# Optimization experiments

Measured on AMD Instinct MI355X. Metric: run time of the kernel, lower is better.

The kernel has to match this reference:

```python
import jax, jax.numpy as jnp
import numpy as np

N = 65536          # total nodes (512 graphs x 128 nodes)
E = 524288         # edges
B = 512            # graphs
D_IN = 128
H_ENC = 256
LAT = 64
H_DEC = 512
NMAX = 128
NP = NMAX * (NMAX - 1) // 2   # 8128 upper-tri pairs
NSTATS = 7
BN_EPS = 1e-5


def _lin(k, i, o):
    return jax.random.normal(k, (i, o), jnp.float32) / np.sqrt(i).astype(np.float32), jnp.zeros((o,), jnp.float32)


def setup_inputs() -> dict:
    key = jax.random.key(0)
    ks = jax.random.split(key, 24)
    inp = {}
    inp['x'] = jax.random.normal(ks[0], (N, D_IN), jnp.float32)
    inp['edge_index'] = jax.random.randint(ks[1], (2, E), 0, N)
    inp['batch'] = jnp.arange(N) // NMAX
    inp['stats'] = jax.random.normal(ks[2], (B, NSTATS), jnp.float32)
    u = jax.random.uniform(ks[3], (B, NP, 2), jnp.float32, 1e-9, 1.0)
    inp['gumbel'] = -jnp.log(-jnp.log(u))
    # GIN conv params (3 layers): Linear -> LeakyReLU -> BN -> Linear -> LeakyReLU
    dims = [(D_IN, H_ENC), (H_ENC, H_ENC), (H_ENC, H_ENC)]
    for li, (di, do) in enumerate(dims):
        w1, b1 = _lin(ks[4 + 2 * li], di, do)
        w2, b2 = _lin(ks[5 + 2 * li], do, do)
        inp[f'cw1_{li}'], inp[f'cb1_{li}'] = w1, b1
        inp[f'cg_{li}'], inp[f'cbe_{li}'] = jnp.ones((do,), jnp.float32), jnp.zeros((do,), jnp.float32)
        inp[f'cw2_{li}'], inp[f'cb2_{li}'] = w2, b2
    # encoder head: BN(hidden+7) -> fc(hidden+7 -> hidden) -> fc_mu(hidden -> latent)
    inp['bn_g'] = jnp.ones((H_ENC + NSTATS,), jnp.float32)
    inp['bn_b'] = jnp.zeros((H_ENC + NSTATS,), jnp.float32)
    inp['fc_w'], inp['fc_b'] = _lin(ks[10], H_ENC + NSTATS, H_ENC)
    inp['mu_w'], inp['mu_b'] = _lin(ks[11], H_ENC, LAT)
    # decoder MLP: (latent+7) -> H_DEC -> H_DEC -> 2*NP
    inp['d0_w'], inp['d0_b'] = _lin(ks[12], LAT + NSTATS, H_DEC)
    inp['d1_w'], inp['d1_b'] = _lin(ks[13], H_DEC, H_DEC)
    inp['d2_w'], inp['d2_b'] = _lin(ks[14], H_DEC, 2 * NP)
    return inp


def _bn_eval(h, g, b):
    # BatchNorm1d in eval mode with default running stats (mean=0, var=1)
    return h * (g / jnp.sqrt(1.0 + BN_EPS)) + b


def _lrelu(h):
    return jnp.where(h > 0, h, 0.2 * h)


def reference(x, edge_index, batch, stats, gumbel,
              cw1_0, cb1_0, cg_0, cbe_0, cw2_0, cb2_0,
              cw1_1, cb1_1, cg_1, cbe_1, cw2_1, cb2_1,
              cw1_2, cb1_2, cg_2, cbe_2, cw2_2, cb2_2,
              bn_g, bn_b, fc_w, fc_b, mu_w, mu_b,
              d0_w, d0_b, d1_w, d1_b, d2_w, d2_b):
    src, dst = edge_index[0], edge_index[1]
    convs = [(cw1_0, cb1_0, cg_0, cbe_0, cw2_0, cb2_0),
             (cw1_1, cb1_1, cg_1, cbe_1, cw2_1, cb2_1),
             (cw1_2, cb1_2, cg_2, cbe_2, cw2_2, cb2_2)]
    h = x
    for w1, b1, g, be, w2, b2 in convs:
        # GINConv (eps=0): nn(x_i + sum_{j->i} x_j) via scatter-add on targets
        agg = h + jax.ops.segment_sum(h[src], dst, num_segments=N)
        t = _lrelu(agg @ w1 + b1)
        t = _bn_eval(t, g, be)
        h = _lrelu(t @ w2 + b2)
        # dropout inactive (eval mode)
    pooled = jax.ops.segment_sum(h, batch, num_segments=B)         # global_add_pool -> [B, H_ENC]
    out = jnp.concatenate([pooled, stats], axis=1)                 # [B, H_ENC+7]
    out = _bn_eval(out, bn_g, bn_b) @ fc_w + fc_b                  # [B, H_ENC]
    mu = out @ mu_w + mu_b                                         # reparameterize (eval) -> mu, [B, LAT]
    z = jnp.concatenate([mu, stats], axis=1)                       # [B, LAT+7] matches decoder input dim
    d = jax.nn.relu(z @ d0_w + d0_b)
    d = jax.nn.relu(d @ d1_w + d1_b)
    logits = (d @ d2_w + d2_b).reshape(B, NP, 2)
    # hard gumbel-softmax (tau=1) with straight-through, keep channel 0
    y = logits + gumbel
    soft = jax.nn.softmax(y, axis=-1)
    hard = jax.nn.one_hot(jnp.argmax(y, axis=-1), 2, dtype=soft.dtype)
    st = hard + soft - jax.lax.stop_gradient(soft)
    vals = st[:, :, 0]                                             # [B, NP]
    iu0, iu1 = jnp.triu_indices(NMAX, k=1)
    adj = jnp.zeros((B, NMAX, NMAX), vals.dtype).at[:, iu0, iu1].set(vals)
    adj = adj + jnp.swapaxes(adj, 1, 2)
    return adj
```

## Files before the change

### kernel.cpp

```cpp
#include <hip/hip_runtime.h>

#define NN 65536
#define NE 524288
#define BG 512
#define DIN 128
#define HE 256
#define LATD 64
#define HD 512
#define NMX 128
#define NPAIR 8128
#define NST 7

__global__ void vae_hist(const int* __restrict__ dst, int* __restrict__ cnt) {
    int e = blockIdx.x * 256 + threadIdx.x;
    if (e < NE) atomicAdd(&cnt[dst[e]], 1);
}

__global__ void vae_scan1(const int* __restrict__ cnt, int* __restrict__ excl, int* __restrict__ bsum) {
    __shared__ int sd[256];
    const int b = blockIdx.x, t = threadIdx.x;
    int v = cnt[b * 256 + t];
    sd[t] = v;
    __syncthreads();
    int acc = v;
    for (int off = 1; off < 256; off <<= 1) {
        int tv = (t >= off) ? sd[t - off] : 0;
        __syncthreads();
        acc += tv;
        sd[t] = acc;
        __syncthreads();
    }
    excl[b * 256 + t] = acc - v;
    if (t == 255) bsum[b] = acc;
}

__global__ void vae_scan2(int* __restrict__ bsum) {
    __shared__ int sd[256];
    const int t = threadIdx.x;
    int v = bsum[t];
    sd[t] = v;
    __syncthreads();
    int acc = v;
    for (int off = 1; off < 256; off <<= 1) {
        int tv = (t >= off) ? sd[t - off] : 0;
        __syncthreads();
        acc += tv;
        sd[t] = acc;
        __syncthreads();
    }
    bsum[t] = acc - v;
}

__global__ void vae_scan3(const int* __restrict__ excl, const int* __restrict__ bsum,
                          int* __restrict__ rs, int* __restrict__ cur) {
    const int i = blockIdx.x * 256 + threadIdx.x;
    const int v = excl[i] + bsum[blockIdx.x];
    rs[i] = v;
    cur[i] = v;
    if (i == NN - 1) rs[NN] = NE;
}

__global__ void vae_fill(const int* __restrict__ dst, int* __restrict__ cur, int* __restrict__ eid) {
    int e = blockIdx.x * 256 + threadIdx.x;
    if (e < NE) {
        int p = atomicAdd(&cur[dst[e]], 1);
        eid[p] = e;
    }
}

__global__ void vae_sort(const int* __restrict__ rs, int* __restrict__ eid,
                         const int* __restrict__ srcarr, int* __restrict__ csrc) {
    int n = blockIdx.x * 256 + threadIdx.x;
    if (n >= NN) return;
    int s = rs[n], e = rs[n + 1];
    for (int a = s + 1; a < e; ++a) {
        int key = eid[a];
        int b = a - 1;
        while (b >= s && eid[b] > key) { eid[b + 1] = eid[b]; --b; }
        eid[b + 1] = key;
    }
    for (int a = s; a < e; ++a) csrc[a] = srcarr[eid[a]];
}

template <int D>
__global__ __launch_bounds__(256) void vae_agg(const float* __restrict__ H,
                                               const int* __restrict__ csrc,
                                               const int* __restrict__ rs,
                                               float* __restrict__ Agg) {
    constexpr int LPG = D / 4;
    const int gid = blockIdx.x * 256 + threadIdx.x;
    const int node = gid / LPG;
    const int lane = gid % LPG;
    if (node >= NN) return;
    float4 acc = *reinterpret_cast<const float4*>(H + (size_t)node * D + lane * 4);
    const int s = rs[node], e = rs[node + 1];
    for (int a = s; a < e; ++a) {
        float4 v = *reinterpret_cast<const float4*>(H + (size_t)csrc[a] * D + lane * 4);
        acc.x += v.x; acc.y += v.y; acc.z += v.z; acc.w += v.w;
    }
    *reinterpret_cast<float4*>(Agg + (size_t)node * D + lane * 4) = acc;
}

template <int K, int EPI>
__global__ __launch_bounds__(256, 2) void vae_sgemm(const float* __restrict__ A,
                                                    const float* __restrict__ W,
                                                    const float* __restrict__ bias,
                                                    const float* __restrict__ g,
                                                    const float* __restrict__ be,
                                                    float* __restrict__ Out) {
    __shared__ float As[32][132];
    __shared__ float Bs[32][264];
    const int tid = threadIdx.x;
    const int tx = tid & 15, ty = tid >> 4;
    const int rowBlk = blockIdx.x * 128;

    float acc[8][16];
#pragma unroll
    for (int r = 0; r < 8; r++)
#pragma unroll
        for (int c = 0; c < 16; c++) acc[r][c] = 0.f;

    const int arow = tid >> 1;
    const int ak = (tid & 1) * 16;
    const float* aptr = A + (size_t)(rowBlk + arow) * K + ak;
    const float* bptr = W + (size_t)ty * HE + tx * 4;

    float4 pa0, pa1, pa2, pa3;
    float4 pb0, pb1, pb2, pb3, pb4, pb5, pb6, pb7;
    auto gload = [&](int ck) {
        const float* an = aptr + ck * 32;
        pa0 = *reinterpret_cast<const float4*>(an);
        pa1 = *reinterpret_cast<const float4*>(an + 4);
        pa2 = *reinterpret_cast<const float4*>(an + 8);
        pa3 = *reinterpret_cast<const float4*>(an + 12);
        const float* bn0 = bptr + (size_t)(ck * 32) * HE;
        pb0 = *reinterpret_cast<const float4*>(bn0);
        pb1 = *reinterpret_cast<const float4*>(bn0 + 64);
        pb2 = *reinterpret_cast<const float4*>(bn0 + 128);
        pb3 = *reinterpret_cast<const float4*>(bn0 + 192);
        const float* bn1 = bn0 + 16 * HE;
        pb4 = *reinterpret_cast<const float4*>(bn1);
        pb5 = *reinterpret_cast<const float4*>(bn1 + 64);
        pb6 = *reinterpret_cast<const float4*>(bn1 + 128);
        pb7 = *reinterpret_cast<const float4*>(bn1 + 192);
    };
    auto swrite = [&]() {
        As[ak + 0][arow] = pa0.x;  As[ak + 1][arow] = pa0.y;
        As[ak + 2][arow] = pa0.z;  As[ak + 3][arow] = pa0.w;
        As[ak + 4][arow] = pa1.x;  As[ak + 5][arow] = pa1.y;
        As[ak + 6][arow] = pa1.z;  As[ak + 7][arow] = pa1.w;
        As[ak + 8][arow] = pa2.x;  As[ak + 9][arow] = pa2.y;
        As[ak + 10][arow] = pa2.z; As[ak + 11][arow] = pa2.w;
        As[ak + 12][arow] = pa3.x; As[ak + 13][arow] = pa3.y;
        As[ak + 14][arow] = pa3.z; As[ak + 15][arow] = pa3.w;
        *reinterpret_cast<float4*>(&Bs[ty][tx * 4]) = pb0;
        *reinterpret_cast<float4*>(&Bs[ty][tx * 4 + 64]) = pb1;
        *reinterpret_cast<float4*>(&Bs[ty][tx * 4 + 128]) = pb2;
        *reinterpret_cast<float4*>(&Bs[ty][tx * 4 + 192]) = pb3;
        *reinterpret_cast<float4*>(&Bs[ty + 16][tx * 4]) = pb4;
        *reinterpret_cast<float4*>(&Bs[ty + 16][tx * 4 + 64]) = pb5;
        *reinterpret_cast<float4*>(&Bs[ty + 16][tx * 4 + 128]) = pb6;
        *reinterpret_cast<float4*>(&Bs[ty + 16][tx * 4 + 192]) = pb7;
    };

    constexpr int NCK = K / 32;
    gload(0);
    for (int ck = 0; ck < NCK; ++ck) {
        __syncthreads();
        swrite();
        __syncthreads();
        if (ck + 1 < NCK) gload(ck + 1);
#pragma unroll 16
        for (int k = 0; k < 32; ++k) {
            float4 a0 = *reinterpret_cast<const float4*>(&As[k][ty * 8]);
            float4 a1 = *reinterpret_cast<const float4*>(&As[k][ty * 8 + 4]);
            float4 b0 = *reinterpret_cast<const float4*>(&Bs[k][tx * 4]);
            float4 b1 = *reinterpret_cast<const float4*>(&Bs[k][tx * 4 + 64]);
            float4 b2 = *reinterpret_cast<const float4*>(&Bs[k][tx * 4 + 128]);
            float4 b3 = *reinterpret_cast<const float4*>(&Bs[k][tx * 4 + 192]);
            float ar[8] = {a0.x, a0.y, a0.z, a0.w, a1.x, a1.y, a1.z, a1.w};
            float bv[16] = {b0.x, b0.y, b0.z, b0.w, b1.x, b1.y, b1.z, b1.w,
                            b2.x, b2.y, b2.z, b2.w, b3.x, b3.y, b3.z, b3.w};
#pragma unroll
            for (int r = 0; r < 8; r++)
#pragma unroll
                for (int c = 0; c < 16; c++)
                    acc[r][c] = fmaf(ar[r], bv[c], acc[r][c]);
        }
    }

    if constexpr (EPI == 2) {
        float psum[16];
#pragma unroll
        for (int c = 0; c < 16; c++) psum[c] = 0.f;
#pragma unroll
        for (int cg = 0; cg < 4; cg++) {
            const int col = cg * 64 + tx * 4;
            float4 bb = *reinterpret_cast<const float4*>(&bias[col]);
            float bbv[4] = {bb.x, bb.y, bb.z, bb.w};
#pragma unroll
            for (int r = 0; r < 8; r++)
#pragma unroll
                for (int c = 0; c < 4; c++) {
                    float t = acc[r][cg * 4 + c] + bbv[c];
                    t = t > 0.f ? t : 0.2f * t;
                    psum[cg * 4 + c] += t;
                }
        }
        __syncthreads();
#pragma unroll
        for (int cg = 0; cg < 4; cg++)
#pragma unroll
            for (int c = 0; c < 4; c++)
                Bs[ty][cg * 64 + tx * 4 + c] = psum[cg * 4 + c];
        __syncthreads();
        float s = 0.f;
#pragma unroll
        for (int k = 0; k < 16; k++) s += Bs[k][tid];
        Out[(size_t)blockIdx.x * HE + tid] = s;
        return;
    }

    const float sq = sqrtf(1.0f + 1e-5f);
#pragma unroll
    for (int cg = 0; cg < 4; cg++) {
        const int col = cg * 64 + tx * 4;
        float4 bb = *reinterpret_cast<const float4*>(&bias[col]);
        float bbv[4] = {bb.x, bb.y, bb.z, bb.w};
        float sc[4], bev[4];
        if constexpr (EPI == 0) {
            float4 gg = *reinterpret_cast<const float4*>(&g[col]);
            float4 ee = *reinterpret_cast<const float4*>(&be[col]);
            sc[0] = gg.x / sq; sc[1] = gg.y / sq; sc[2] = gg.z / sq; sc[3] = gg.w / sq;
            bev[0] = ee.x; bev[1] = ee.y; bev[2] = ee.z; bev[3] = ee.w;
        }
#pragma unroll
        for (int r = 0; r < 8; r++) {
            const int row = rowBlk + ty * 8 + r;
            float o[4];
#pragma unroll
            for (int c = 0; c < 4; c++) {
                float t = acc[r][cg * 4 + c] + bbv[c];
                t = t > 0.f ? t : 0.2f * t;
                if constexpr (EPI == 0) t = t * sc[c] + bev[c];
                o[c] = t;
            }
            *reinterpret_cast<float4*>(Out + (size_t)row * HE + col) =
                *reinterpret_cast<float4*>(&o[0]);
        }
    }
}

__global__ __launch_bounds__(256) void vae_pooldec(const float* __restrict__ pooled, const float* __restrict__ stats,
                                                   const float* __restrict__ bng, const float* __restrict__ bnb,
                                                   const float* __restrict__ fcw, const float* __restrict__ fcb,
                                                   const float* __restrict__ muw, const float* __restrict__ mub,
                                                   const float* __restrict__ d0w, const float* __restrict__ d0b,
                                                   const float* __restrict__ d1w, const float* __restrict__ d1b,
                                                   float* __restrict__ Dm) {
    __shared__ float vin[264];
    __shared__ float fo[256];
    __shared__ float z[72];
    __shared__ float dd[512];
    const int b = blockIdx.x, t = threadIdx.x;

    const float sq = sqrtf(1.0f + 1e-5f);
    float m0 = pooled[(size_t)b * HE + t] * (bng[t] / sq) + bnb[t];
    vin[t] = m0;
    if (t < NST) vin[HE + t] = stats[b * NST + t] * (bng[HE + t] / sq) + bnb[HE + t];
    __syncthreads();

    float a = fcb[t];
    for (int k = 0; k < HE + NST; k++) a = fmaf(vin[k], fcw[(size_t)k * HE + t], a);
    fo[t] = a;
    __syncthreads();

    if (t < LATD) {
        float m = mub[t];
        for (int k = 0; k < HE; k++) m = fmaf(fo[k], muw[(size_t)k * LATD + t], m);
        z[t] = m;
    }
    if (t >= LATD && t < LATD + NST) z[t] = stats[b * NST + (t - LATD)];
    __syncthreads();

    float a0 = d0b[t], a1 = d0b[t + 256];
    for (int k = 0; k < LATD + NST; k++) {
        float zk = z[k];
        a0 = fmaf(zk, d0w[(size_t)k * HD + t], a0);
        a1 = fmaf(zk, d0w[(size_t)k * HD + t + 256], a1);
    }
    dd[t] = a0 > 0.f ? a0 : 0.f;
    dd[t + 256] = a1 > 0.f ? a1 : 0.f;
    __syncthreads();

    float c0 = d1b[t], c1 = d1b[t + 256];
    for (int k = 0; k < HD; k++) {
        float dk = dd[k];
        c0 = fmaf(dk, d1w[(size_t)k * HD + t], c0);
        c1 = fmaf(dk, d1w[(size_t)k * HD + t + 256], c1);
    }
    Dm[(size_t)b * HD + t] = c0 > 0.f ? c0 : 0.f;
    Dm[(size_t)b * HD + t + 256] = c1 > 0.f ? c1 : 0.f;
}

__global__ void vae_pairdiff(const float* __restrict__ In, float* __restrict__ Od) {
    int gidx = blockIdx.x * 256 + threadIdx.x;
    int r = gidx >> 11, pq = gidx & 2047;
    float4 o;
    o.x = 0.f; o.y = 0.f; o.z = 0.f; o.w = 0.f;
    if (pq < 2032) {
        const float* s = In + (size_t)r * (2 * NPAIR) + pq * 8;
        float4 u = *reinterpret_cast<const float4*>(s);
        float4 v = *reinterpret_cast<const float4*>(s + 4);
        o.x = u.x - u.y; o.y = u.z - u.w; o.z = v.x - v.y; o.w = v.z - v.w;
    }
    *reinterpret_cast<float4*>(Od + (size_t)r * 8192 + pq * 4) = o;
}

__global__ __launch_bounds__(256, 4) void vae_d2gemm(const float* __restrict__ A,
                                                     const float* __restrict__ Wd,
                                                     const float* __restrict__ Bb,
                                                     float* __restrict__ Gd) {
    __shared__ float As[16][132];
    __shared__ float Bs[16][68];
    const int tid = threadIdx.x;
    const int tx = tid & 15, ty = tid >> 4;
    const int rowBlk = blockIdx.y * 128, colBlk = blockIdx.x * 64;

    float acc[8][4];
#pragma unroll
    for (int r = 0; r < 8; r++)
#pragma unroll
        for (int c = 0; c < 4; c++) acc[r][c] = 0.f;

    const int arow = tid >> 1;
    const int ak = (tid & 1) * 8;
    const float* aptr = A + (size_t)(rowBlk + arow) * HD + ak;
    const int bk = tid >> 4;
    const int bc = (tid & 15) * 4;
    const float* bptr = Wd + (size_t)bk * 8192 + colBlk + bc;

    float4 pa0 = *reinterpret_cast<const float4*>(aptr);
    float4 pa1 = *reinterpret_cast<const float4*>(aptr + 4);
    float4 pb = *reinterpret_cast<const float4*>(bptr);

    constexpr int NCK = HD / 16;
    for (int ck = 0; ck < NCK; ++ck) {
        __syncthreads();
        As[ak + 0][arow] = pa0.x;
        As[ak + 1][arow] = pa0.y;
        As[ak + 2][arow] = pa0.z;
        As[ak + 3][arow] = pa0.w;
        As[ak + 4][arow] = pa1.x;
        As[ak + 5][arow] = pa1.y;
        As[ak + 6][arow] = pa1.z;
        As[ak + 7][arow] = pa1.w;
        *reinterpret_cast<float4*>(&Bs[bk][bc]) = pb;
        __syncthreads();
        if (ck + 1 < NCK) {
            const float* an = aptr + (ck + 1) * 16;
            pa0 = *reinterpret_cast<const float4*>(an);
            pa1 = *reinterpret_cast<const float4*>(an + 4);
            pb = *reinterpret_cast<const float4*>(bptr + (size_t)(ck + 1) * 16 * 8192);
        }
#pragma unroll
        for (int k = 0; k < 16; ++k) {
            float4 a0 = *reinterpret_cast<const float4*>(&As[k][ty * 8]);
            float4 a1 = *reinterpret_cast<const float4*>(&As[k][ty * 8 + 4]);
            float4 b = *reinterpret_cast<const float4*>(&Bs[k][tx * 4]);
            float ar[8] = {a0.x, a0.y, a0.z, a0.w, a1.x, a1.y, a1.z, a1.w};
            float bv[4] = {b.x, b.y, b.z, b.w};
#pragma unroll
            for (int r = 0; r < 8; r++)
#pragma unroll
                for (int c = 0; c < 4; c++)
                    acc[r][c] = fmaf(ar[r], bv[c], acc[r][c]);
        }
    }

    const int col = colBlk + tx * 4;
    if (col < NPAIR) {
        const float* bp = Bb + 2 * col;
        float4 u = *reinterpret_cast<const float4*>(bp);
        float4 v = *reinterpret_cast<const float4*>(bp + 4);
        float bd[4] = {u.x - u.y, u.z - u.w, v.x - v.y, v.z - v.w};
#pragma unroll
        for (int r = 0; r < 8; r++) {
            const int b_ = rowBlk + ty * 8 + r;
            float* gp = Gd + (size_t)b_ * 8192 + col;
            float4 gv = *reinterpret_cast<const float4*>(gp);
            float gvv[4] = {gv.x, gv.y, gv.z, gv.w};
            float o[4];
#pragma unroll
            for (int c = 0; c < 4; c++) {
                float y = acc[r][c] + bd[c] + gvv[c];
                o[c] = (y >= 0.f) ? 1.0f : 0.0f;
            }
            *reinterpret_cast<float4*>(gp) = *reinterpret_cast<float4*>(&o[0]);
        }
    }
}

__global__ __launch_bounds__(256) void vae_scatter(const float* __restrict__ vals, float* __restrict__ Out) {
    __shared__ float sv[8192];
    const int b = blockIdx.x, t = threadIdx.x;
    const float* vp = vals + (size_t)b * 8192;
#pragma unroll
    for (int i = 0; i < 8; ++i)
        *reinterpret_cast<float4*>(&sv[(i * 256 + t) * 4]) =
            *reinterpret_cast<const float4*>(&vp[(i * 256 + t) * 4]);
    __syncthreads();
    float* op = Out + (size_t)b * (NMX * NMX);
#pragma unroll
    for (int it = 0; it < 16; ++it) {
        int pos = (it * 256 + t) * 4;
        int i = pos >> 7, j0 = pos & 127;
        float o[4];
#pragma unroll
        for (int e = 0; e < 4; ++e) {
            int j = j0 + e;
            float v;
            if (i == j) v = 0.f;
            else if (i < j) v = sv[((i * (255 - i)) >> 1) + j - i - 1];
            else v = sv[((j * (255 - j)) >> 1) + i - j - 1];
            o[e] = v;
        }
        *reinterpret_cast<float4*>(&op[pos]) = *reinterpret_cast<float4*>(&o[0]);
    }
}

extern "C" void kernel_launch(void* const* d_in, const int* in_sizes, int n_in,
                              void* d_out, int out_size, void* d_ws, size_t ws_size,
                              hipStream_t stream) {
    const float* x = (const float*)d_in[0];
    const int* ei = (const int*)d_in[1];
    const float* stats = (const float*)d_in[3];
    const float* gum = (const float*)d_in[4];
    const float* cw1[3] = {(const float*)d_in[5], (const float*)d_in[11], (const float*)d_in[17]};
    const float* cb1[3] = {(const float*)d_in[6], (const float*)d_in[12], (const float*)d_in[18]};
    const float* cg[3] = {(const float*)d_in[7], (const float*)d_in[13], (const float*)d_in[19]};
    const float* cbe[3] = {(const float*)d_in[8], (const float*)d_in[14], (const float*)d_in[20]};
    const float* cw2[3] = {(const float*)d_in[9], (const float*)d_in[15], (const float*)d_in[21]};
    const float* cb2[3] = {(const float*)d_in[10], (const float*)d_in[16], (const float*)d_in[22]};
    const float* bng = (const float*)d_in[23];
    const float* bnb = (const float*)d_in[24];
    const float* fcw = (const float*)d_in[25];
    const float* fcb = (const float*)d_in[26];
    const float* muw = (const float*)d_in[27];
    const float* mub = (const float*)d_in[28];
    const float* d0w = (const float*)d_in[29];
    const float* d0b = (const float*)d_in[30];
    const float* d1w = (const float*)d_in[31];
    const float* d1b = (const float*)d_in[32];
    const float* d2w = (const float*)d_in[33];
    const float* d2b = (const float*)d_in[34];
    float* Out = (float*)d_out;

    char* wp = (char*)d_ws;
    auto alloc = [&](size_t bytes) -> void* {
        void* p = (void*)wp;
        wp += (bytes + 255) & ~(size_t)255;
        return p;
    };
    float* hA = (float*)alloc((size_t)NN * HE * 4);
    float* hB = (float*)alloc((size_t)NN * HE * 4);
    int* cnt = (int*)alloc((size_t)NN * 4);
    int* rs = (int*)alloc((size_t)(NN + 64) * 4);
    int* cur = (int*)alloc((size_t)NN * 4);
    int* eid = (int*)alloc((size_t)NE * 4);
    int* csrc = (int*)alloc((size_t)NE * 4);
    int* bsum = (int*)alloc((size_t)256 * 4);
    float* Dm = (float*)alloc((size_t)BG * HD * 4);
    float* pooled = (float*)alloc((size_t)BG * HE * 4);

    float* wdiff = hA;
    float* gdiff = hA + (size_t)HD * 8192;

    const int* srcArr = ei;
    const int* dstArr = ei + NE;

    hipMemsetAsync(cnt, 0, (size_t)NN * 4, stream);
    vae_hist<<<NE / 256, 256, 0, stream>>>(dstArr, cnt);
    vae_scan1<<<NN / 256, 256, 0, stream>>>(cnt, cur, bsum);
    vae_scan2<<<1, 256, 0, stream>>>(bsum);
    vae_scan3<<<NN / 256, 256, 0, stream>>>(cur, bsum, rs, cur);
    vae_fill<<<NE / 256, 256, 0, stream>>>(dstArr, cur, eid);
    vae_sort<<<NN / 256, 256, 0, stream>>>(rs, eid, srcArr, csrc);

    vae_agg<DIN><<<(NN * 32) / 256, 256, 0, stream>>>(x, csrc, rs, hB);
    vae_sgemm<DIN, 0><<<NN / 128, 256, 0, stream>>>(hB, cw1[0], cb1[0], cg[0], cbe[0], hA);
    vae_sgemm<HE, 1><<<NN / 128, 256, 0, stream>>>(hA, cw2[0], cb2[0], nullptr, nullptr, hB);
    vae_agg<HE><<<(NN * 64) / 256, 256, 0, stream>>>(hB, csrc, rs, hA);
    vae_sgemm<HE, 0><<<NN / 128, 256, 0, stream>>>(hA, cw1[1], cb1[1], cg[1], cbe[1], hB);
    vae_sgemm<HE, 1><<<NN / 128, 256, 0, stream>>>(hB, cw2[1], cb2[1], nullptr, nullptr, hA);
    vae_agg<HE><<<(NN * 64) / 256, 256, 0, stream>>>(hA, csrc, rs, hB);
    vae_sgemm<HE, 0><<<NN / 128, 256, 0, stream>>>(hB, cw1[2], cb1[2], cg[2], cbe[2], hA);
    vae_sgemm<HE, 2><<<NN / 128, 256, 0, stream>>>(hA, cw2[2], cb2[2], nullptr, nullptr, pooled);

    vae_pooldec<<<BG, 256, 0, stream>>>(pooled, stats, bng, bnb, fcw, fcb, muw, mub, d0w, d0b, d1w, d1b, Dm);

    vae_pairdiff<<<(512 * 2048) / 256, 256, 0, stream>>>(d2w, wdiff);
    vae_pairdiff<<<(512 * 2048) / 256, 256, 0, stream>>>(gum, gdiff);
    vae_d2gemm<<<dim3(8192 / 64, BG / 128), 256, 0, stream>>>(Dm, wdiff, d2b, gdiff);
    vae_scatter<<<BG, 256, 0, stream>>>(gdiff, Out);
}
```

Measured before the change: 1.038 ms.

## Fuse GIN neighbor aggregation into first-layer GEMM A-tile loads

Removes the separate aggregation kernel and computes each node's neighbor sum while loading its A tile into shared memory inside the first GEMM of each GIN layer. This drops the write and re-read of the aggregated activation buffer and three kernel launches. In exchange, the gather runs inside the GEMM prefetch with per-thread loops of varying length, so load imbalance and gather latency can stall the GEMM pipeline. The second GEMM's BN epilogue parameters are also removed, since that path never used them.

```diff
diff --git a/kernel.cpp b/kernel.cpp
--- a/kernel.cpp
+++ b/kernel.cpp
@@ -82,31 +82,139 @@
     for (int a = s; a < e; ++a) csrc[a] = srcarr[eid[a]];
 }
 
-template <int D>
-__global__ __launch_bounds__(256) void vae_agg(const float* __restrict__ H,
-                                               const int* __restrict__ csrc,
-                                               const int* __restrict__ rs,
-                                               float* __restrict__ Agg) {
-    constexpr int LPG = D / 4;
-    const int gid = blockIdx.x * 256 + threadIdx.x;
-    const int node = gid / LPG;
-    const int lane = gid % LPG;
-    if (node >= NN) return;
-    float4 acc = *reinterpret_cast<const float4*>(H + (size_t)node * D + lane * 4);
-    const int s = rs[node], e = rs[node + 1];
-    for (int a = s; a < e; ++a) {
-        float4 v = *reinterpret_cast<const float4*>(H + (size_t)csrc[a] * D + lane * 4);
-        acc.x += v.x; acc.y += v.y; acc.z += v.z; acc.w += v.w;
-    }
-    *reinterpret_cast<float4*>(Agg + (size_t)node * D + lane * 4) = acc;
+template <int K>
+__global__ __launch_bounds__(256, 2) void vae_gemm1f(const float* __restrict__ Hm,
+                                                     const int* __restrict__ rs,
+                                                     const int* __restrict__ csrc,
+                                                     const float* __restrict__ W,
+                                                     const float* __restrict__ bias,
+                                                     const float* __restrict__ g,
+                                                     const float* __restrict__ be,
+                                                     float* __restrict__ Out) {
+    __shared__ float As[32][132];
+    __shared__ float Bs[32][264];
+    const int tid = threadIdx.x;
+    const int tx = tid & 15, ty = tid >> 4;
+    const int rowBlk = blockIdx.x * 128;
+
+    float acc[8][16];
+#pragma unroll
+    for (int r = 0; r < 8; r++)
+#pragma unroll
+        for (int c = 0; c < 16; c++) acc[r][c] = 0.f;
+
+    const int arow = tid >> 1;
+    const int ak = (tid & 1) * 16;
+    const int row = rowBlk + arow;
+    const int s0 = rs[row], e0 = rs[row + 1];
+    const float* aown = Hm + (size_t)row * K + ak;
+    const float* bptr = W + (size_t)ty * HE + tx * 4;
+
+    float4 pa0, pa1, pa2, pa3;
+    float4 pb0, pb1, pb2, pb3, pb4, pb5, pb6, pb7;
+    auto gload = [&](int ck) {
+        const float* an = aown + ck * 32;
+        pa0 = *reinterpret_cast<const float4*>(an);
+        pa1 = *reinterpret_cast<const float4*>(an + 4);
+        pa2 = *reinterpret_cast<const float4*>(an + 8);
+        pa3 = *reinterpret_cast<const float4*>(an + 12);
+        for (int a = s0; a < e0; ++a) {
+            const float* nb = Hm + (size_t)csrc[a] * K + ak + ck * 32;
+            float4 n0 = *reinterpret_cast<const float4*>(nb);
+            float4 n1 = *reinterpret_cast<const float4*>(nb + 4);
+            float4 n2 = *reinterpret_cast<const float4*>(nb + 8);
+            float4 n3 = *reinterpret_cast<const float4*>(nb + 12);
+            pa0.x += n0.x; pa0.y += n0.y; pa0.z += n0.z; pa0.w += n0.w;
+            pa1.x += n1.x; pa1.y += n1.y; pa1.z += n1.z; pa1.w += n1.w;
+            pa2.x += n2.x; pa2.y += n2.y; pa2.z += n2.z; pa2.w += n2.w;
+            pa3.x += n3.x; pa3.y += n3.y; pa3.z += n3.z; pa3.w += n3.w;
+        }
+        const float* bn0 = bptr + (size_t)(ck * 32) * HE;
+        pb0 = *reinterpret_cast<const float4*>(bn0);
+        pb1 = *reinterpret_cast<const float4*>(bn0 + 64);
+        pb2 = *reinterpret_cast<const float4*>(bn0 + 128);
+        pb3 = *reinterpret_cast<const float4*>(bn0 + 192);
+        const float* bn1 = bn0 + 16 * HE;
+        pb4 = *reinterpret_cast<const float4*>(bn1);
+        pb5 = *reinterpret_cast<const float4*>(bn1 + 64);
+        pb6 = *reinterpret_cast<const float4*>(bn1 + 128);
+        pb7 = *reinterpret_cast<const float4*>(bn1 + 192);
+    };
+    auto swrite = [&]() {
+        As[ak + 0][arow] = pa0.x;  As[ak + 1][arow] = pa0.y;
+        As[ak + 2][arow] = pa0.z;  As[ak + 3][arow] = pa0.w;
+        As[ak + 4][arow] = pa1.x;  As[ak + 5][arow] = pa1.y;
+        As[ak + 6][arow] = pa1.z;  As[ak + 7][arow] = pa1.w;
+        As[ak + 8][arow] = pa2.x;  As[ak + 9][arow] = pa2.y;
+        As[ak + 10][arow] = pa2.z; As[ak + 11][arow] = pa2.w;
+        As[ak + 12][arow] = pa3.x; As[ak + 13][arow] = pa3.y;
+        As[ak + 14][arow] = pa3.z; As[ak + 15][arow] = pa3.w;
+        *reinterpret_cast<float4*>(&Bs[ty][tx * 4]) = pb0;
+        *reinterpret_cast<float4*>(&Bs[ty][tx * 4 + 64]) = pb1;
+        *reinterpret_cast<float4*>(&Bs[ty][tx * 4 + 128]) = pb2;
+        *reinterpret_cast<float4*>(&Bs[ty][tx * 4 + 192]) = pb3;
+        *reinterpret_cast<float4*>(&Bs[ty + 16][tx * 4]) = pb4;
+        *reinterpret_cast<float4*>(&Bs[ty + 16][tx * 4 + 64]) = pb5;
+        *reinterpret_cast<float4*>(&Bs[ty + 16][tx * 4 + 128]) = pb6;
+        *reinterpret_cast<float4*>(&Bs[ty + 16][tx * 4 + 192]) = pb7;
+    };
+
+    constexpr int NCK = K / 32;
+    gload(0);
+    for (int ck = 0; ck < NCK; ++ck) {
+        __syncthreads();
+        swrite();
+        __syncthreads();
+        if (ck + 1 < NCK) gload(ck + 1);
+#pragma unroll 16
+        for (int k = 0; k < 32; ++k) {
+            float4 a0 = *reinterpret_cast<const float4*>(&As[k][ty * 8]);
+            float4 a1 = *reinterpret_cast<const float4*>(&As[k][ty * 8 + 4]);
+            float4 b0 = *reinterpret_cast<const float4*>(&Bs[k][tx * 4]);
+            float4 b1 = *reinterpret_cast<const float4*>(&Bs[k][tx * 4 + 64]);
+            float4 b2 = *reinterpret_cast<const float4*>(&Bs[k][tx * 4 + 128]);
+            float4 b3 = *reinterpret_cast<const float4*>(&Bs[k][tx * 4 + 192]);
+            float ar[8] = {a0.x, a0.y, a0.z, a0.w, a1.x, a1.y, a1.z, a1.w};
+            float bv[16] = {b0.x, b0.y, b0.z, b0.w, b1.x, b1.y, b1.z, b1.w,
+                            b2.x, b2.y, b2.z, b2.w, b3.x, b3.y, b3.z, b3.w};
+#pragma unroll
+            for (int r = 0; r < 8; r++)
+#pragma unroll
+                for (int c = 0; c < 16; c++)
+                    acc[r][c] = fmaf(ar[r], bv[c], acc[r][c]);
+        }
+    }
+
+    const float sq = sqrtf(1.0f + 1e-5f);
+#pragma unroll
+    for (int cg = 0; cg < 4; cg++) {
+        const int col = cg * 64 + tx * 4;
+        float4 bb = *reinterpret_cast<const float4*>(&bias[col]);
+        float4 gg = *reinterpret_cast<const float4*>(&g[col]);
+        float4 ee = *reinterpret_cast<const float4*>(&be[col]);
+        float bbv[4] = {bb.x, bb.y, bb.z, bb.w};
+        float sc[4] = {gg.x / sq, gg.y / sq, gg.z / sq, gg.w / sq};
+        float bev[4] = {ee.x, ee.y, ee.z, ee.w};
+#pragma unroll
+        for (int r = 0; r < 8; r++) {
+            const int orow = rowBlk + ty * 8 + r;
+            float o[4];
+#pragma unroll
+            for (int c = 0; c < 4; c++) {
+                float t = acc[r][cg * 4 + c] + bbv[c];
+                t = t > 0.f ? t : 0.2f * t;
+                o[c] = t * sc[c] + bev[c];
+            }
+            *reinterpret_cast<float4*>(Out + (size_t)orow * HE + col) =
+                *reinterpret_cast<float4*>(&o[0]);
+        }
+    }
 }
 
 template <int K, int EPI>
 __global__ __launch_bounds__(256, 2) void vae_sgemm(const float* __restrict__ A,
                                                     const float* __restrict__ W,
                                                     const float* __restrict__ bias,
-                                                    const float* __restrict__ g,
-                                                    const float* __restrict__ be,
                                                     float* __restrict__ Out) {
     __shared__ float As[32][132];
     __shared__ float Bs[32][264];
@@ -221,19 +329,11 @@
         return;
     }
 
-    const float sq = sqrtf(1.0f + 1e-5f);
 #pragma unroll
     for (int cg = 0; cg < 4; cg++) {
         const int col = cg * 64 + tx * 4;
         float4 bb = *reinterpret_cast<const float4*>(&bias[col]);
         float bbv[4] = {bb.x, bb.y, bb.z, bb.w};
-        float sc[4], bev[4];
-        if constexpr (EPI == 0) {
-            float4 gg = *reinterpret_cast<const float4*>(&g[col]);
-            float4 ee = *reinterpret_cast<const float4*>(&be[col]);
-            sc[0] = gg.x / sq; sc[1] = gg.y / sq; sc[2] = gg.z / sq; sc[3] = gg.w / sq;
-            bev[0] = ee.x; bev[1] = ee.y; bev[2] = ee.z; bev[3] = ee.w;
-        }
 #pragma unroll
         for (int r = 0; r < 8; r++) {
             const int row = rowBlk + ty * 8 + r;
@@ -241,9 +341,7 @@
 #pragma unroll
             for (int c = 0; c < 4; c++) {
                 float t = acc[r][cg * 4 + c] + bbv[c];
-                t = t > 0.f ? t : 0.2f * t;
-                if constexpr (EPI == 0) t = t * sc[c] + bev[c];
-                o[c] = t;
+                o[c] = t > 0.f ? t : 0.2f * t;
             }
             *reinterpret_cast<float4*>(Out + (size_t)row * HE + col) =
                 *reinterpret_cast<float4*>(&o[0]);
@@ -487,15 +585,12 @@
     vae_fill<<<NE / 256, 256, 0, stream>>>(dstArr, cur, eid);
     vae_sort<<<NN / 256, 256, 0, stream>>>(rs, eid, srcArr, csrc);
 
-    vae_agg<DIN><<<(NN * 32) / 256, 256, 0, stream>>>(x, csrc, rs, hB);
-    vae_sgemm<DIN, 0><<<NN / 128, 256, 0, stream>>>(hB, cw1[0], cb1[0], cg[0], cbe[0], hA);
-    vae_sgemm<HE, 1><<<NN / 128, 256, 0, stream>>>(hA, cw2[0], cb2[0], nullptr, nullptr, hB);
-    vae_agg<HE><<<(NN * 64) / 256, 256, 0, stream>>>(hB, csrc, rs, hA);
-    vae_sgemm<HE, 0><<<NN / 128, 256, 0, stream>>>(hA, cw1[1], cb1[1], cg[1], cbe[1], hB);
-    vae_sgemm<HE, 1><<<NN / 128, 256, 0, stream>>>(hB, cw2[1], cb2[1], nullptr, nullptr, hA);
-    vae_agg<HE><<<(NN * 64) / 256, 256, 0, stream>>>(hA, csrc, rs, hB);
-    vae_sgemm<HE, 0><<<NN / 128, 256, 0, stream>>>(hB, cw1[2], cb1[2], cg[2], cbe[2], hA);
-    vae_sgemm<HE, 2><<<NN / 128, 256, 0, stream>>>(hA, cw2[2], cb2[2], nullptr, nullptr, pooled);
+    vae_gemm1f<DIN><<<NN / 128, 256, 0, stream>>>(x, rs, csrc, cw1[0], cb1[0], cg[0], cbe[0], hA);
+    vae_sgemm<HE, 1><<<NN / 128, 256, 0, stream>>>(hA, cw2[0], cb2[0], hB);
+    vae_gemm1f<HE><<<NN / 128, 256, 0, stream>>>(hB, rs, csrc, cw1[1], cb1[1], cg[1], cbe[1], hA);
+    vae_sgemm<HE, 1><<<NN / 128, 256, 0, stream>>>(hA, cw2[1], cb2[1], hB);
+    vae_gemm1f<HE><<<NN / 128, 256, 0, stream>>>(hB, rs, csrc, cw1[2], cb1[2], cg[2], cbe[2], hA);
+    vae_sgemm<HE, 2><<<NN / 128, 256, 0, stream>>>(hA, cw2[2], cb2[2], pooled);
 
     vae_pooldec<<<BG, 256, 0, stream>>>(pooled, stats, bng, bnb, fcw, fcb, muw, mub, d0w, d0b, d1w, d1b, Dm);
 
```

New measurement: 1.023 ms. About the same (-1.4%).
